# Kernel tuning notes

Hardware: AMD Instinct MI355X
Metric: run time of the kernel (lower is better)

The kernel has to match this reference:

```python
import jax, jax.numpy as jnp
import numpy as np

LOG2 = float(np.log(2.0))


def setup_inputs() -> dict:
    key = jax.random.key(0)
    k1, k2, k3, k4, k5, k6 = jax.random.split(key, 6)
    N, E, G = 50000, 800000, 256
    d_node, d_edge, d_global, hidden = 128, 64, 64, 128
    node_feats = jax.random.normal(k1, (N, d_node), dtype=jnp.float32)
    edge_feats = jax.random.normal(k2, (E, d_edge), dtype=jnp.float32)
    global_feats = jax.random.normal(k3, (G, d_global), dtype=jnp.float32)
    edge_index = jax.random.randint(k4, (2, E), 0, N, dtype=jnp.int64)
    batch = jnp.sort(jax.random.randint(k5, (N,), 0, G, dtype=jnp.int64))
    # Linear(384 -> 128, bias=False); torch stores weight as [out, in], apply x @ W.T
    d_in = 2 * d_node + d_edge + d_global
    W = jax.random.normal(k6, (hidden, d_in), dtype=jnp.float32) * (1.0 / np.sqrt(d_in))
    return {"node_feats": node_feats, "edge_feats": edge_feats,
            "global_feats": global_feats, "edge_index": edge_index,
            "batch": batch, "W": W}


def reference(node_feats, edge_feats, global_feats, edge_index, batch, W):
    idx_src = edge_index[0]
    idx_dst = edge_index[1]
    batch_edge_map = batch[idx_src]                      # [E]
    out = jnp.concatenate([
        node_feats[idx_src],                             # [E, d_node]
        node_feats[idx_dst],                             # [E, d_node]
        edge_feats,                                      # [E, d_edge]
        global_feats[batch_edge_map],                    # [E, d_global]
    ], axis=1)                                           # [E, 384]
    h = out @ W.T                                        # [E, hidden]
    return jax.nn.softplus(h) - LOG2                     # shifted softplus
```

## Files before the change

### kernel.cpp

```cpp
#include <hip/hip_runtime.h>
#include <hip/hip_bf16.h>

#define N_NODES 50000
#define N_EDGES 800000
#define D_NODE  128
#define D_EDGE  64
#define D_GLOB  64
#define D_IN    384
#define D_OUT   128
#define LN2F    0.69314718055994531f

#define APITCH  392

typedef __attribute__((ext_vector_type(4))) float  floatx4;
typedef __attribute__((ext_vector_type(8))) short  shortx8;

#define MFMA16 __builtin_amdgcn_mfma_f32_16x16x32_bf16

__device__ __forceinline__ shortx8 cvt8_bf16(const float* __restrict__ p) {
    floatx4 a = *(const floatx4*)p;
    floatx4 b = *(const floatx4*)(p + 4);
    shortx8 r;
    union { __hip_bfloat16 h; short s; } u;
    #pragma unroll
    for (int j = 0; j < 4; ++j) {
        u.h = __float2bfloat16(a[j]); r[j]     = u.s;
        u.h = __float2bfloat16(b[j]); r[j + 4] = u.s;
    }
    return r;
}

__global__ __launch_bounds__(256, 2)
void proj_node_kernel(const float* __restrict__ node,
                      const float* __restrict__ W,
                      float* __restrict__ Psrc,
                      float* __restrict__ Pdst)
{
    const int bid   = blockIdx.x;
    const int table = bid & 1;
    const int i0    = (bid >> 1) * 64;
    float* __restrict__ P = table ? Pdst : Psrc;
    const int coloff = table * D_NODE;

    const int tid  = threadIdx.x;
    const int wave = tid >> 6;
    const int lane = tid & 63;
    const int nlo  = lane & 15;
    const int quad = lane >> 4;

    shortx8 wfrag[2][4];
    #pragma unroll
    for (int nt = 0; nt < 2; ++nt) {
        const int n = wave * 32 + nt * 16 + nlo;
        #pragma unroll
        for (int kc = 0; kc < 4; ++kc)
            wfrag[nt][kc] = cvt8_bf16(W + (size_t)n * D_IN + coloff + kc * 32 + quad * 8);
    }

    floatx4 acc[2][4];
    #pragma unroll
    for (int nt = 0; nt < 2; ++nt)
        #pragma unroll
        for (int it = 0; it < 4; ++it)
            acc[nt][it] = (floatx4){0.f, 0.f, 0.f, 0.f};

    #pragma unroll
    for (int kc = 0; kc < 4; ++kc) {
        #pragma unroll
        for (int it = 0; it < 4; ++it) {
            int i = i0 + it * 16 + nlo;
            if (i >= N_NODES) i = N_NODES - 1;
            shortx8 b = cvt8_bf16(node + (size_t)i * D_NODE + kc * 32 + quad * 8);
            acc[0][it] = MFMA16(wfrag[0][kc], b, acc[0][it], 0, 0, 0);
            acc[1][it] = MFMA16(wfrag[1][kc], b, acc[1][it], 0, 0, 0);
        }
    }

    #pragma unroll
    for (int it = 0; it < 4; ++it) {
        const int i = i0 + it * 16 + nlo;
        if (i < N_NODES) {
            #pragma unroll
            for (int nt = 0; nt < 2; ++nt) {
                const int n0 = wave * 32 + nt * 16 + quad * 4;
                *(floatx4*)(P + (size_t)i * D_OUT + n0) = acc[nt][it];
            }
        }
    }
}

__global__ __launch_bounds__(256, 2)
void proj_glob_kernel(const float* __restrict__ globf,
                      const float* __restrict__ W,
                      float* __restrict__ Pglob)
{
    const int i0   = blockIdx.x * 64;
    const int tid  = threadIdx.x;
    const int wave = tid >> 6;
    const int lane = tid & 63;
    const int nlo  = lane & 15;
    const int quad = lane >> 4;

    shortx8 wfrag[2][2];
    #pragma unroll
    for (int nt = 0; nt < 2; ++nt) {
        const int n = wave * 32 + nt * 16 + nlo;
        #pragma unroll
        for (int kc = 0; kc < 2; ++kc)
            wfrag[nt][kc] = cvt8_bf16(W + (size_t)n * D_IN + 320 + kc * 32 + quad * 8);
    }

    floatx4 acc[2][4];
    #pragma unroll
    for (int nt = 0; nt < 2; ++nt)
        #pragma unroll
        for (int it = 0; it < 4; ++it)
            acc[nt][it] = (floatx4){0.f, 0.f, 0.f, 0.f};

    #pragma unroll
    for (int kc = 0; kc < 2; ++kc) {
        #pragma unroll
        for (int it = 0; it < 4; ++it) {
            const int i = i0 + it * 16 + nlo;
            shortx8 b = cvt8_bf16(globf + (size_t)i * D_GLOB + kc * 32 + quad * 8);
            acc[0][it] = MFMA16(wfrag[0][kc], b, acc[0][it], 0, 0, 0);
            acc[1][it] = MFMA16(wfrag[1][kc], b, acc[1][it], 0, 0, 0);
        }
    }

    #pragma unroll
    for (int it = 0; it < 4; ++it) {
        const int i = i0 + it * 16 + nlo;
        #pragma unroll
        for (int nt = 0; nt < 2; ++nt) {
            const int n0 = wave * 32 + nt * 16 + quad * 4;
            *(floatx4*)(Pglob + (size_t)i * D_OUT + n0) = acc[nt][it];
        }
    }
}

__global__ __launch_bounds__(256, 2)
void edge_fused_kernel(const float* __restrict__ edgef,
                       const int* __restrict__ eidx,
                       const int* __restrict__ batch,
                       const float* __restrict__ W,
                       const float* __restrict__ Psrc,
                       const float* __restrict__ Pdst,
                       const float* __restrict__ Pglob,
                       float* __restrict__ out)
{
    const int tid  = threadIdx.x;
    const int e0   = blockIdx.x * 64;
    const int wave = tid >> 6;
    const int lane = tid & 63;
    const int nlo  = lane & 15;
    const int quad = lane >> 4;

    const int is64 = ((eidx[1] | eidx[3] | eidx[5] | eidx[7] |
                       eidx[9] | eidx[11] | eidx[13] | eidx[15]) == 0) ? 1 : 0;

    int src[4], dst[4], bat[4];
    #pragma unroll
    for (int et = 0; et < 4; ++et) {
        const int e = e0 + et * 16 + nlo;
        src[et] = eidx[(size_t)e << is64];
        dst[et] = eidx[(size_t)(N_EDGES + e) << is64];
    }
    #pragma unroll
    for (int et = 0; et < 4; ++et)
        bat[et] = batch[(size_t)src[et] << is64];

    shortx8 bfrag[4][2];
    #pragma unroll
    for (int et = 0; et < 4; ++et) {
        const float* row = edgef + (size_t)(e0 + et * 16 + nlo) * D_EDGE;
        #pragma unroll
        for (int kc = 0; kc < 2; ++kc)
            bfrag[et][kc] = cvt8_bf16(row + kc * 32 + quad * 8);
    }

    shortx8 wfrag[2][2];
    #pragma unroll
    for (int nt = 0; nt < 2; ++nt) {
        const int n = wave * 32 + nt * 16 + nlo;
        #pragma unroll
        for (int kc = 0; kc < 2; ++kc)
            wfrag[nt][kc] = cvt8_bf16(W + (size_t)n * D_IN + 256 + kc * 32 + quad * 8);
    }

    floatx4 acc[2][4];
    #pragma unroll
    for (int nt = 0; nt < 2; ++nt)
        #pragma unroll
        for (int et = 0; et < 4; ++et)
            acc[nt][et] = (floatx4){0.f, 0.f, 0.f, 0.f};

    #pragma unroll
    for (int kc = 0; kc < 2; ++kc) {
        #pragma unroll
        for (int et = 0; et < 4; ++et) {
            acc[0][et] = MFMA16(wfrag[0][kc], bfrag[et][kc], acc[0][et], 0, 0, 0);
            acc[1][et] = MFMA16(wfrag[1][kc], bfrag[et][kc], acc[1][et], 0, 0, 0);
        }
    }

    #pragma unroll
    for (int et = 0; et < 4; ++et) {
        const int e = e0 + et * 16 + nlo;
        const float* ps = Psrc  + (size_t)src[et] * D_OUT;
        const float* pd = Pdst  + (size_t)dst[et] * D_OUT;
        const float* pg = Pglob + (size_t)bat[et] * D_OUT;
        #pragma unroll
        for (int nt = 0; nt < 2; ++nt) {
            const int n0 = wave * 32 + nt * 16 + quad * 4;
            floatx4 g1 = *(const floatx4*)(ps + n0);
            floatx4 g2 = *(const floatx4*)(pd + n0);
            floatx4 g3 = *(const floatx4*)(pg + n0);
            floatx4 r;
            #pragma unroll
            for (int j = 0; j < 4; ++j) {
                const float h = acc[nt][et][j] + g1[j] + g2[j] + g3[j];
                const float t = __expf(-fabsf(h));
                r[j] = fmaxf(h, 0.f) + __logf(1.f + t) - LN2F;
            }
            __builtin_nontemporal_store(r, (floatx4*)(out + (size_t)e * D_OUT + n0));
        }
    }
}

__global__ __launch_bounds__(256, 2)
void edge_mlp_kernel(const float* __restrict__ node,
                     const float* __restrict__ edgef,
                     const float* __restrict__ globf,
                     const int* __restrict__ eidx,
                     const int* __restrict__ batch,
                     const float* __restrict__ W,
                     float* __restrict__ out)
{
    __shared__ short A_lds[64 * APITCH];

    const int tid = threadIdx.x;
    const int e0  = blockIdx.x * 64;

    const int is64 = ((eidx[1] | eidx[3] | eidx[5] | eidx[7] |
                       eidx[9] | eidx[11] | eidx[13] | eidx[15]) == 0) ? 1 : 0;

    #pragma unroll
    for (int i = 0; i < 12; ++i) {
        int g       = tid + i * 256;
        int e_local = g / 48;
        int off     = (g - e_local * 48) * 8;
        int e       = e0 + e_local;
        const float* srcp;
        if (off < 128) {
            int s = eidx[(size_t)e << is64];
            srcp = node + (size_t)s * D_NODE + off;
        } else if (off < 256) {
            int d = eidx[(size_t)(N_EDGES + e) << is64];
            srcp = node + (size_t)d * D_NODE + (off - 128);
        } else if (off < 320) {
            srcp = edgef + (size_t)e * D_EDGE + (off - 256);
        } else {
            int s = eidx[(size_t)e << is64];
            int b = batch[(size_t)s << is64];
            srcp = globf + (size_t)b * D_GLOB + (off - 320);
        }
        *(shortx8*)(&A_lds[e_local * APITCH + off]) = cvt8_bf16(srcp);
    }

    const int wave = tid >> 6;
    const int lane = tid & 63;
    const int nlo  = lane & 15;
    const int quad = lane >> 4;

    shortx8 bfrag[12][2];
    #pragma unroll
    for (int kc = 0; kc < 12; ++kc) {
        #pragma unroll
        for (int nt = 0; nt < 2; ++nt) {
            int n = wave * 32 + nt * 16 + nlo;
            bfrag[kc][nt] = cvt8_bf16(W + (size_t)n * D_IN + kc * 32 + quad * 8);
        }
    }

    floatx4 acc[4][2];
    #pragma unroll
    for (int mt = 0; mt < 4; ++mt)
        #pragma unroll
        for (int nt = 0; nt < 2; ++nt)
            acc[mt][nt] = (floatx4){0.f, 0.f, 0.f, 0.f};

    __syncthreads();

    #pragma unroll
    for (int kc = 0; kc < 12; ++kc) {
        #pragma unroll
        for (int mt = 0; mt < 4; ++mt) {
            shortx8 afrag = *(const shortx8*)(
                &A_lds[(mt * 16 + nlo) * APITCH + kc * 32 + quad * 8]);
            #pragma unroll
            for (int nt = 0; nt < 2; ++nt) {
                acc[mt][nt] = MFMA16(afrag, bfrag[kc][nt], acc[mt][nt], 0, 0, 0);
            }
        }
    }

    #pragma unroll
    for (int mt = 0; mt < 4; ++mt) {
        #pragma unroll
        for (int nt = 0; nt < 2; ++nt) {
            int n = wave * 32 + nt * 16 + nlo;
            #pragma unroll
            for (int r = 0; r < 4; ++r) {
                int e = e0 + mt * 16 + quad * 4 + r;
                float h  = acc[mt][nt][r];
                float t  = __expf(-fabsf(h));
                float sp = fmaxf(h, 0.0f) + __logf(1.0f + t);
                out[(size_t)e * D_OUT + n] = sp - LN2F;
            }
        }
    }
}

extern "C" void kernel_launch(void* const* d_in, const int* in_sizes, int n_in,
                              void* d_out, int out_size, void* d_ws, size_t ws_size,
                              hipStream_t stream) {
    const float* node  = (const float*)d_in[0];
    const float* edgef = (const float*)d_in[1];
    const float* globf = (const float*)d_in[2];
    const int*   eidx  = (const int*)d_in[3];
    const int*   batch = (const int*)d_in[4];
    const float* W     = (const float*)d_in[5];
    float*       out   = (float*)d_out;

    const size_t PN   = (size_t)N_NODES * D_OUT;
    const size_t need = (2 * PN + 256 * D_OUT) * sizeof(float);

    if (ws_size >= need) {
        float* Psrc  = (float*)d_ws;
        float* Pdst  = Psrc + PN;
        float* Pglob = Pdst + PN;
        proj_node_kernel<<<dim3(782 * 2), dim3(256), 0, stream>>>(node, W, Psrc, Pdst);
        proj_glob_kernel<<<dim3(4), dim3(256), 0, stream>>>(globf, W, Pglob);
        edge_fused_kernel<<<dim3(N_EDGES / 64), dim3(256), 0, stream>>>(
            edgef, eidx, batch, W, Psrc, Pdst, Pglob, out);
    } else {
        edge_mlp_kernel<<<dim3(N_EDGES / 64), dim3(256), 0, stream>>>(
            node, edgef, globf, eidx, batch, W, out);
    }
}
```

Baseline: 872.8 us.

## Fold global projection into per-node source table and prefetch gathered rows

The global-feature projection is now added into the source-node projection table inside the node projection kernel, using batch[src]. This removes the per-edge batch lookup and the third gathered row in the edge kernel. The edge kernel also issues its Psrc/Pdst gathers early, uses them to initialise the MFMA accumulators, reads edge features with nontemporal loads, and raises the occupancy hint to 3 blocks. The cost is a small extra gather in the node kernel, a fixed kernel ordering (global before node), and higher register pressure from holding the prefetched rows.

```diff
diff --git a/kernel.cpp b/kernel.cpp
--- a/kernel.cpp
+++ b/kernel.cpp
@@ -30,63 +30,17 @@
     return r;
 }
 
-__global__ __launch_bounds__(256, 2)
-void proj_node_kernel(const float* __restrict__ node,
-                      const float* __restrict__ W,
-                      float* __restrict__ Psrc,
-                      float* __restrict__ Pdst)
-{
-    const int bid   = blockIdx.x;
-    const int table = bid & 1;
-    const int i0    = (bid >> 1) * 64;
-    float* __restrict__ P = table ? Pdst : Psrc;
-    const int coloff = table * D_NODE;
-
-    const int tid  = threadIdx.x;
-    const int wave = tid >> 6;
-    const int lane = tid & 63;
-    const int nlo  = lane & 15;
-    const int quad = lane >> 4;
-
-    shortx8 wfrag[2][4];
-    #pragma unroll
-    for (int nt = 0; nt < 2; ++nt) {
-        const int n = wave * 32 + nt * 16 + nlo;
-        #pragma unroll
-        for (int kc = 0; kc < 4; ++kc)
-            wfrag[nt][kc] = cvt8_bf16(W + (size_t)n * D_IN + coloff + kc * 32 + quad * 8);
-    }
-
-    floatx4 acc[2][4];
-    #pragma unroll
-    for (int nt = 0; nt < 2; ++nt)
-        #pragma unroll
-        for (int it = 0; it < 4; ++it)
-            acc[nt][it] = (floatx4){0.f, 0.f, 0.f, 0.f};
-
-    #pragma unroll
-    for (int kc = 0; kc < 4; ++kc) {
-        #pragma unroll
-        for (int it = 0; it < 4; ++it) {
-            int i = i0 + it * 16 + nlo;
-            if (i >= N_NODES) i = N_NODES - 1;
-            shortx8 b = cvt8_bf16(node + (size_t)i * D_NODE + kc * 32 + quad * 8);
-            acc[0][it] = MFMA16(wfrag[0][kc], b, acc[0][it], 0, 0, 0);
-            acc[1][it] = MFMA16(wfrag[1][kc], b, acc[1][it], 0, 0, 0);
-        }
-    }
-
-    #pragma unroll
-    for (int it = 0; it < 4; ++it) {
-        const int i = i0 + it * 16 + nlo;
-        if (i < N_NODES) {
-            #pragma unroll
-            for (int nt = 0; nt < 2; ++nt) {
-                const int n0 = wave * 32 + nt * 16 + quad * 4;
-                *(floatx4*)(P + (size_t)i * D_OUT + n0) = acc[nt][it];
-            }
-        }
-    }
+__device__ __forceinline__ shortx8 cvt8_bf16_nt(const float* __restrict__ p) {
+    floatx4 a = __builtin_nontemporal_load((const floatx4*)p);
+    floatx4 b = __builtin_nontemporal_load((const floatx4*)(p + 4));
+    shortx8 r;
+    union { __hip_bfloat16 h; short s; } u;
+    #pragma unroll
+    for (int j = 0; j < 4; ++j) {
+        u.h = __float2bfloat16(a[j]); r[j]     = u.s;
+        u.h = __float2bfloat16(b[j]); r[j + 4] = u.s;
+    }
+    return r;
 }
 
 __global__ __launch_bounds__(256, 2)
@@ -140,13 +94,92 @@
 }
 
 __global__ __launch_bounds__(256, 2)
+void proj_node_kernel(const float* __restrict__ node,
+                      const float* __restrict__ W,
+                      const int* __restrict__ eidx,
+                      const int* __restrict__ batch,
+                      const float* __restrict__ Pglob,
+                      float* __restrict__ Psrc,
+                      float* __restrict__ Pdst)
+{
+    const int bid   = blockIdx.x;
+    const int table = bid & 1;
+    const int i0    = (bid >> 1) * 64;
+    float* __restrict__ P = table ? Pdst : Psrc;
+    const int coloff = table * D_NODE;
+
+    const int tid  = threadIdx.x;
+    const int wave = tid >> 6;
+    const int lane = tid & 63;
+    const int nlo  = lane & 15;
+    const int quad = lane >> 4;
+
+    const int is64 = ((eidx[1] | eidx[3] | eidx[5] | eidx[7] |
+                       eidx[9] | eidx[11] | eidx[13] | eidx[15]) == 0) ? 1 : 0;
+
+    shortx8 wfrag[2][4];
+    #pragma unroll
+    for (int nt = 0; nt < 2; ++nt) {
+        const int n = wave * 32 + nt * 16 + nlo;
+        #pragma unroll
+        for (int kc = 0; kc < 4; ++kc)
+            wfrag[nt][kc] = cvt8_bf16(W + (size_t)n * D_IN + coloff + kc * 32 + quad * 8);
+    }
+
+    floatx4 acc[2][4];
+    #pragma unroll
+    for (int nt = 0; nt < 2; ++nt)
+        #pragma unroll
+        for (int it = 0; it < 4; ++it)
+            acc[nt][it] = (floatx4){0.f, 0.f, 0.f, 0.f};
+
+    #pragma unroll
+    for (int kc = 0; kc < 4; ++kc) {
+        #pragma unroll
+        for (int it = 0; it < 4; ++it) {
+            int i = i0 + it * 16 + nlo;
+            if (i >= N_NODES) i = N_NODES - 1;
+            shortx8 b = cvt8_bf16(node + (size_t)i * D_NODE + kc * 32 + quad * 8);
+            acc[0][it] = MFMA16(wfrag[0][kc], b, acc[0][it], 0, 0, 0);
+            acc[1][it] = MFMA16(wfrag[1][kc], b, acc[1][it], 0, 0, 0);
+        }
+    }
+
+    if (table == 0) {
+        #pragma unroll
+        for (int it = 0; it < 4; ++it) {
+            const int i = i0 + it * 16 + nlo;
+            if (i < N_NODES) {
+                const int b = batch[(size_t)i << is64];
+                const float* pg = Pglob + (size_t)b * D_OUT;
+                #pragma unroll
+                for (int nt = 0; nt < 2; ++nt) {
+                    const int n0 = wave * 32 + nt * 16 + quad * 4;
+                    acc[nt][it] += *(const floatx4*)(pg + n0);
+                }
+            }
+        }
+    }
+
+    #pragma unroll
+    for (int it = 0; it < 4; ++it) {
+        const int i = i0 + it * 16 + nlo;
+        if (i < N_NODES) {
+            #pragma unroll
+            for (int nt = 0; nt < 2; ++nt) {
+                const int n0 = wave * 32 + nt * 16 + quad * 4;
+                *(floatx4*)(P + (size_t)i * D_OUT + n0) = acc[nt][it];
+            }
+        }
+    }
+}
+
+__global__ __launch_bounds__(256, 3)
 void edge_fused_kernel(const float* __restrict__ edgef,
                        const int* __restrict__ eidx,
-                       const int* __restrict__ batch,
                        const float* __restrict__ W,
                        const float* __restrict__ Psrc,
                        const float* __restrict__ Pdst,
-                       const float* __restrict__ Pglob,
                        float* __restrict__ out)
 {
     const int tid  = threadIdx.x;
@@ -159,16 +192,26 @@
     const int is64 = ((eidx[1] | eidx[3] | eidx[5] | eidx[7] |
                        eidx[9] | eidx[11] | eidx[13] | eidx[15]) == 0) ? 1 : 0;
 
-    int src[4], dst[4], bat[4];
+    int src[4], dst[4];
     #pragma unroll
     for (int et = 0; et < 4; ++et) {
         const int e = e0 + et * 16 + nlo;
         src[et] = eidx[(size_t)e << is64];
         dst[et] = eidx[(size_t)(N_EDGES + e) << is64];
     }
-    #pragma unroll
-    for (int et = 0; et < 4; ++et)
-        bat[et] = batch[(size_t)src[et] << is64];
+
+    floatx4 gs[4][2], gd[4][2];
+    #pragma unroll
+    for (int et = 0; et < 4; ++et) {
+        const float* ps = Psrc + (size_t)src[et] * D_OUT;
+        const float* pd = Pdst + (size_t)dst[et] * D_OUT;
+        #pragma unroll
+        for (int nt = 0; nt < 2; ++nt) {
+            const int n0 = wave * 32 + nt * 16 + quad * 4;
+            gs[et][nt] = *(const floatx4*)(ps + n0);
+            gd[et][nt] = *(const floatx4*)(pd + n0);
+        }
+    }
 
     shortx8 bfrag[4][2];
     #pragma unroll
@@ -176,7 +219,7 @@
         const float* row = edgef + (size_t)(e0 + et * 16 + nlo) * D_EDGE;
         #pragma unroll
         for (int kc = 0; kc < 2; ++kc)
-            bfrag[et][kc] = cvt8_bf16(row + kc * 32 + quad * 8);
+            bfrag[et][kc] = cvt8_bf16_nt(row + kc * 32 + quad * 8);
     }
 
     shortx8 wfrag[2][2];
@@ -193,7 +236,7 @@
     for (int nt = 0; nt < 2; ++nt)
         #pragma unroll
         for (int et = 0; et < 4; ++et)
-            acc[nt][et] = (floatx4){0.f, 0.f, 0.f, 0.f};
+            acc[nt][et] = gs[et][nt] + gd[et][nt];
 
     #pragma unroll
     for (int kc = 0; kc < 2; ++kc) {
@@ -207,19 +250,13 @@
     #pragma unroll
     for (int et = 0; et < 4; ++et) {
         const int e = e0 + et * 16 + nlo;
-        const float* ps = Psrc  + (size_t)src[et] * D_OUT;
-        const float* pd = Pdst  + (size_t)dst[et] * D_OUT;
-        const float* pg = Pglob + (size_t)bat[et] * D_OUT;
         #pragma unroll
         for (int nt = 0; nt < 2; ++nt) {
             const int n0 = wave * 32 + nt * 16 + quad * 4;
-            floatx4 g1 = *(const floatx4*)(ps + n0);
-            floatx4 g2 = *(const floatx4*)(pd + n0);
-            floatx4 g3 = *(const floatx4*)(pg + n0);
             floatx4 r;
             #pragma unroll
             for (int j = 0; j < 4; ++j) {
-                const float h = acc[nt][et][j] + g1[j] + g2[j] + g3[j];
+                const float h = acc[nt][et][j];
                 const float t = __expf(-fabsf(h));
                 r[j] = fmaxf(h, 0.f) + __logf(1.f + t) - LN2F;
             }
@@ -340,10 +377,11 @@
         float* Psrc  = (float*)d_ws;
         float* Pdst  = Psrc + PN;
         float* Pglob = Pdst + PN;
-        proj_node_kernel<<<dim3(782 * 2), dim3(256), 0, stream>>>(node, W, Psrc, Pdst);
         proj_glob_kernel<<<dim3(4), dim3(256), 0, stream>>>(globf, W, Pglob);
+        proj_node_kernel<<<dim3(782 * 2), dim3(256), 0, stream>>>(
+            node, W, eidx, batch, Pglob, Psrc, Pdst);
         edge_fused_kernel<<<dim3(N_EDGES / 64), dim3(256), 0, stream>>>(
-            edgef, eidx, batch, W, Psrc, Pdst, Pglob, out);
+            edgef, eidx, W, Psrc, Pdst, out);
     } else {
         edge_mlp_kernel<<<dim3(N_EDGES / 64), dim3(256), 0, stream>>>(
             node, edgef, globf, eidx, batch, W, out);
```

After: 892.0 us. 1.02x slower.
